# Kernel tuning notes

Hardware: AMD Instinct MI355X
Metric: run time of the kernel (lower is better)

## Reference

```python
import jax, jax.numpy as jnp
import numpy as np

B, N, K, D = 32, 100, 20, 4096
DI = 512   # img_feat_dim
DO = 512   # obj_feat_dim (must equal DI for the module to run)
H = 512    # lstm_hidden_dim
L = 2      # n_hidden_layers


def _w(key, shape, fan_in):
    return (jax.random.normal(key, shape, jnp.float32) / np.sqrt(fan_in)).astype(jnp.float32)


def setup_inputs() -> dict:
    key = jax.random.key(0)
    ks = jax.random.split(key, 24)
    inp = {
        "x": jax.random.normal(ks[0], (B, N, K, D), jnp.float32),
        # feature linears
        "W_img": _w(ks[1], (DI, D), D), "b_img": jnp.zeros((DI,), jnp.float32),
        "W_obj": _w(ks[2], (DO, D), D), "b_obj": jnp.zeros((DO,), jnp.float32),
        "W_obj2": _w(ks[3], (DI, DO), DO), "b_obj2": jnp.zeros((DI,), jnp.float32),
        # Fattn (no biases)
        "W_ah": _w(ks[4], (DI, H), H),   # hidden_linear: H -> DI
        "W_ac": _w(ks[5], (1, DI), DI),  # combined_linear: DI -> 1
        # LSTM layer 0 (input 2*DI) and layer 1 (input H); PyTorch gate order i,f,g,o
        "W_ih0": _w(ks[6], (4 * H, DI + DO), DI + DO), "W_hh0": _w(ks[7], (4 * H, H), H),
        "b_ih0": jnp.zeros((4 * H,), jnp.float32), "b_hh0": jnp.zeros((4 * H,), jnp.float32),
        "W_ih1": _w(ks[8], (4 * H, H), H), "W_hh1": _w(ks[9], (4 * H, H), H),
        "b_ih1": jnp.zeros((4 * H,), jnp.float32), "b_hh1": jnp.zeros((4 * H,), jnp.float32),
        # output head
        "W_out": _w(ks[10], (1, H), H), "b_out": jnp.zeros((1,), jnp.float32),
    }
    return inp


def _forward(x, W_img, b_img, W_obj, b_obj, W_obj2, b_obj2, W_ah, W_ac,
             W_ih0, W_hh0, b_ih0, b_hh0, W_ih1, W_hh1, b_ih1, b_hh1, W_out, b_out):
    Bx, Nx, Kx, Dx = x.shape
    # obj_mask: (B, N, K-1, 1)
    obj_mask = jnp.sum(x[:, :, 1:], axis=-1, keepdims=True)
    img_feat = x[:, :, 0, :] @ W_img.T + b_img                      # (B, N, DI)
    obj_feat = (x[:, :, 1:, :] @ W_obj.T + b_obj) * obj_mask        # (B, N, K-1, DO)
    obj_feat = obj_feat @ W_obj2.T + b_obj2                         # (B, N, K-1, DI)

    lstm_params = ((W_ih0, W_hh0, b_ih0, b_hh0), (W_ih1, W_hh1, b_ih1, b_hh1))

    def step(carry, inp):
        h, c, prev = carry                 # h,c: (L,B,H); prev: (B,H) = top-layer output
        a, im, m = inp                     # a:(B,K-1,DI) im:(B,DI) m:(B,K-1,1)
        # Fattn: note softmax over a size-1 axis -> ones; kept for faithfulness
        hprime = (prev @ W_ah.T)[:, None, :]                        # (B,1,DI)
        e = jnp.tanh(hprime + a)
        al = e @ W_ac.T                                             # (B,K-1,1)
        al = jax.nn.softmax(al, axis=-1) * m                        # == m
        w_obj = jnp.sum(a * al, axis=1)                             # (B,DI)
        xl = jnp.concatenate([im, w_obj], axis=1)                   # (B, DI+DO)
        hs, cs = [], []
        for l, (Wih, Whh, bih, bhh) in enumerate(lstm_params):
            g = xl @ Wih.T + bih + h[l] @ Whh.T + bhh
            gi, gf, gg, go = jnp.split(g, 4, axis=-1)
            cn = jax.nn.sigmoid(gf) * c[l] + jax.nn.sigmoid(gi) * jnp.tanh(gg)
            hn = jax.nn.sigmoid(go) * jnp.tanh(cn)
            hs.append(hn); cs.append(cn); xl = hn
        h = jnp.stack(hs); c = jnp.stack(cs)
        pred = xl @ W_out.T + b_out                                 # (B,1)
        return (h, c, xl), (al, pred[:, 0])

    h0 = jnp.zeros((L, Bx, H), x.dtype)
    c0 = jnp.zeros_like(h0)
    p0 = jnp.zeros((Bx, H), x.dtype)
    xs = (obj_feat.transpose(1, 0, 2, 3), img_feat.transpose(1, 0, 2),
          obj_mask.transpose(1, 0, 2, 3))
    _, (alphas, preds) = jax.lax.scan(step, (h0, c0, p0), xs)
    # alphas: (N, B, K-1, 1) (torch returns a list of N); preds -> (B, N) like torch.cat dim=1
    return alphas, preds.T


def reference(x, W_img, b_img, W_obj, b_obj, W_obj2, b_obj2, W_ah, W_ac,
              W_ih0, W_hh0, b_ih0, b_hh0, W_ih1, W_hh1, b_ih1, b_hh1, W_out, b_out):
    return _forward(x, W_img, b_img, W_obj, b_obj, W_obj2, b_obj2, W_ah, W_ac,
                    W_ih0, W_hh0, b_ih0, b_hh0, W_ih1, W_hh1, b_ih1, b_hh1, W_out, b_out)
```

## Files before the change

### kernel.cpp

```cpp
#include <hip/hip_runtime.h>


__device__ __forceinline__ float sigf(float x) { return 1.0f / (1.0f + __expf(-x)); }

__global__ __launch_bounds__(256) void mask_z_kernel(
    const float* __restrict__ x, float* __restrict__ z,
    float* __restrict__ s1, float* __restrict__ s2, float* __restrict__ alphas)
{
  int m = blockIdx.x;
  int b = m / 100, n = m % 100;
  int t = threadIdx.x;
  const float* xb = x + (size_t)m * 81920;
  __shared__ float red[4];
  float zv[16];
#pragma unroll
  for (int i = 0; i < 16; ++i) zv[i] = 0.f;
  float s1v = 0.f, s2v = 0.f;
  for (int k = 1; k < 20; ++k) {
    const float4* row = (const float4*)(xb + (size_t)k * 4096);
    float4 v0 = row[t], v1 = row[t + 256], v2 = row[t + 512], v3 = row[t + 768];
    float ps = v0.x + v0.y + v0.z + v0.w + v1.x + v1.y + v1.z + v1.w
             + v2.x + v2.y + v2.z + v2.w + v3.x + v3.y + v3.z + v3.w;
#pragma unroll
    for (int off = 32; off >= 1; off >>= 1) ps += __shfl_down(ps, off);
    if ((t & 63) == 0) red[t >> 6] = ps;
    __syncthreads();
    float mk = red[0] + red[1] + red[2] + red[3];
    __syncthreads();
    float mk2 = mk * mk;
    s1v += mk; s2v += mk2;
    if (t == 0) alphas[((size_t)n * 32 + (size_t)b) * 19 + (k - 1)] = mk;
    zv[0] += mk2 * v0.x; zv[1] += mk2 * v0.y; zv[2] += mk2 * v0.z; zv[3] += mk2 * v0.w;
    zv[4] += mk2 * v1.x; zv[5] += mk2 * v1.y; zv[6] += mk2 * v1.z; zv[7] += mk2 * v1.w;
    zv[8] += mk2 * v2.x; zv[9] += mk2 * v2.y; zv[10] += mk2 * v2.z; zv[11] += mk2 * v2.w;
    zv[12] += mk2 * v3.x; zv[13] += mk2 * v3.y; zv[14] += mk2 * v3.z; zv[15] += mk2 * v3.w;
  }
  float4* zr = (float4*)(z + (size_t)m * 4096);
  zr[t]       = make_float4(zv[0], zv[1], zv[2], zv[3]);
  zr[t + 256] = make_float4(zv[4], zv[5], zv[6], zv[7]);
  zr[t + 512] = make_float4(zv[8], zv[9], zv[10], zv[11]);
  zr[t + 768] = make_float4(zv[12], zv[13], zv[14], zv[15]);
  if (t == 0) { s1[m] = s1v; s2[m] = s2v; }
}

__global__ void colvec_kernel(const float* __restrict__ W2,
                              const float* __restrict__ bo, float* __restrict__ vb)
{
  int j = blockIdx.x * 256 + threadIdx.x;
  if (j < 512) {
    float s = 0.f;
    for (int i = 0; i < 512; ++i) s += W2[(size_t)j * 512 + i] * bo[i];
    vb[j] = s;
  }
}

__global__ __launch_bounds__(256) void gemm_atb(
    const float* __restrict__ A, int lda,
    const float* __restrict__ W, int K,
    float* __restrict__ C, int ldc,
    const float* __restrict__ bias1, const float* __restrict__ bias2,
    const float* __restrict__ rs1, const float* __restrict__ cv1,
    const float* __restrict__ rs2, const float* __restrict__ cv2)
{
  __shared__ __align__(16) float As[32 * 76];
  __shared__ __align__(16) float Ws[32 * 76];
  int t = threadIdx.x;
  int m0 = blockIdx.x * 64, n0 = blockIdx.y * 64;
  int sr = t >> 3;
  int sc = t & 7;
  int r0 = (t >> 4) * 4, c0 = (t & 15) * 4;

  float acc[4][4];
#pragma unroll
  for (int i = 0; i < 4; ++i)
#pragma unroll
    for (int j = 0; j < 4; ++j) acc[i][j] = 0.f;

  const float* Ap0 = A + (size_t)(m0 + sr) * lda + sc * 4;
  const float* Ap1 = A + (size_t)(m0 + sr + 32) * lda + sc * 4;
  const float* Wp0 = W + (size_t)(n0 + sr) * K + sc * 4;
  const float* Wp1 = W + (size_t)(n0 + sr + 32) * K + sc * 4;

  float4 a0 = *(const float4*)(Ap0);
  float4 a1 = *(const float4*)(Ap1);
  float4 w0 = *(const float4*)(Wp0);
  float4 w1 = *(const float4*)(Wp1);

  for (int k0 = 0; k0 < K; k0 += 32) {
    int kb = sc * 4;
#pragma unroll
    for (int j = 0; j < 4; ++j) {
      float aj0 = (j == 0) ? a0.x : (j == 1) ? a0.y : (j == 2) ? a0.z : a0.w;
      float aj1 = (j == 0) ? a1.x : (j == 1) ? a1.y : (j == 2) ? a1.z : a1.w;
      float wj0 = (j == 0) ? w0.x : (j == 1) ? w0.y : (j == 2) ? w0.z : w0.w;
      float wj1 = (j == 0) ? w1.x : (j == 1) ? w1.y : (j == 2) ? w1.z : w1.w;
      As[(kb + j) * 76 + sr]      = aj0;
      As[(kb + j) * 76 + sr + 32] = aj1;
      Ws[(kb + j) * 76 + sr]      = wj0;
      Ws[(kb + j) * 76 + sr + 32] = wj1;
    }
    __syncthreads();
    if (k0 + 32 < K) {
      a0 = *(const float4*)(Ap0 + k0 + 32);
      a1 = *(const float4*)(Ap1 + k0 + 32);
      w0 = *(const float4*)(Wp0 + k0 + 32);
      w1 = *(const float4*)(Wp1 + k0 + 32);
    }
#pragma unroll 8
    for (int kk = 0; kk < 32; ++kk) {
      float4 av = *(const float4*)&As[kk * 76 + r0];
      float4 wv = *(const float4*)&Ws[kk * 76 + c0];
      float ar[4] = {av.x, av.y, av.z, av.w};
      float wr[4] = {wv.x, wv.y, wv.z, wv.w};
#pragma unroll
      for (int i = 0; i < 4; ++i)
#pragma unroll
        for (int j = 0; j < 4; ++j) acc[i][j] += ar[i] * wr[j];
    }
    __syncthreads();
  }
#pragma unroll
  for (int i = 0; i < 4; ++i) {
    int m = m0 + r0 + i;
    float r1v = rs1 ? rs1[m] : 0.f;
    float r2v = rs2 ? rs2[m] : 0.f;
#pragma unroll
    for (int j = 0; j < 4; ++j) {
      int n = n0 + c0 + j;
      float v = acc[i][j];
      if (bias1) v += bias1[n];
      if (bias2) v += bias2[n];
      if (cv1) v += r1v * cv1[n];
      if (cv2) v += r2v * cv2[n];
      C[(size_t)m * ldc + n] = v;
    }
  }
}

__global__ __launch_bounds__(256) void lstm_phase(
    const float* __restrict__ gin,
    const float* __restrict__ Whh0,
    const float* __restrict__ Wih1,
    const float* __restrict__ Whh1,
    const float* __restrict__ b_ih1, const float* __restrict__ b_hh1,
    const float* __restrict__ Wout, const float* __restrict__ bout,
    const float* __restrict__ hA_prev, const float* __restrict__ cA_prev,
    float* __restrict__ hA_cur, float* __restrict__ cA_cur,
    const float* __restrict__ h1_prev, const float* __restrict__ c1_prev,
    float* __restrict__ h1_cur, float* __restrict__ c1_cur,
    float* __restrict__ preds, int p)
{
  __shared__ __align__(16) float lds[8 * 1024 + 1024];
  int bid = blockIdx.x, t = threadIdx.x;
  bool isA = bid < 256;
  int wg = isA ? bid : bid - 256;

  {
    int r = t >> 5, c = t & 31;
    int grow = (r >> 1) * 512 + wg * 2 + (r & 1);
    if (isA) {
      const float4* src = (const float4*)(Whh0 + (size_t)grow * 512);
#pragma unroll
      for (int i = 0; i < 4; ++i) {
        int k4 = i * 32 + c;
        *(float4*)&lds[r * 512 + ((k4 ^ r) << 2)] = src[k4];
      }
    } else {
      const float4* sih = (const float4*)(Wih1 + (size_t)grow * 512);
      const float4* shh = (const float4*)(Whh1 + (size_t)grow * 512);
#pragma unroll
      for (int i = 0; i < 8; ++i) {
        int k4g = i * 32 + c;
        int half = k4g >> 7;
        int k4 = k4g & 127;
        float4 v = half ? shh[k4] : sih[k4];
        *(float4*)&lds[r * 1024 + half * 512 + ((k4 ^ r) << 2)] = v;
      }
    }
  }
  __syncthreads();

  bool active = isA ? (p <= 99) : (p >= 1 && p <= 100);
  int tc = t & 7, bg = (t >> 3) & 7, ks = t >> 6;
  int b0 = bg * 4;
  float a0 = 0.f, a1 = 0.f, a2 = 0.f, a3 = 0.f;

  if (active) {
    if (isA) {
      int base = tc * 512;
      const float* h = hA_prev;
#pragma unroll 4
      for (int kk = 0; kk < 32; ++kk) {
        int k4 = ks * 32 + kk;
        float4 w = *(const float4*)&lds[base + ((k4 ^ tc) << 2)];
        const float* hp = h + k4 * 4;
        float4 h0v = *(const float4*)(hp + (b0 + 0) * 512);
        float4 h1v = *(const float4*)(hp + (b0 + 1) * 512);
        float4 h2v = *(const float4*)(hp + (b0 + 2) * 512);
        float4 h3v = *(const float4*)(hp + (b0 + 3) * 512);
        a0 += w.x * h0v.x + w.y * h0v.y + w.z * h0v.z + w.w * h0v.w;
        a1 += w.x * h1v.x + w.y * h1v.y + w.z * h1v.z + w.w * h1v.w;
        a2 += w.x * h2v.x + w.y * h2v.y + w.z * h2v.z + w.w * h2v.w;
        a3 += w.x * h3v.x + w.y * h3v.y + w.z * h3v.z + w.w * h3v.w;
      }
    } else {
      int half = ks >> 1;
      const float* xv = half ? h1_prev : hA_prev;
      int base = tc * 1024 + half * 512;
#pragma unroll 4
      for (int kk = 0; kk < 64; ++kk) {
        int k4 = (ks & 1) * 64 + kk;
        float4 w = *(const float4*)&lds[base + ((k4 ^ tc) << 2)];
        const float* hp = xv + k4 * 4;
        float4 h0v = *(const float4*)(hp + (b0 + 0) * 512);
        float4 h1v = *(const float4*)(hp + (b0 + 1) * 512);
        float4 h2v = *(const float4*)(hp + (b0 + 2) * 512);
        float4 h3v = *(const float4*)(hp + (b0 + 3) * 512);
        a0 += w.x * h0v.x + w.y * h0v.y + w.z * h0v.z + w.w * h0v.w;
        a1 += w.x * h1v.x + w.y * h1v.y + w.z * h1v.z + w.w * h1v.w;
        a2 += w.x * h2v.x + w.y * h2v.y + w.z * h2v.z + w.w * h2v.w;
        a3 += w.x * h3v.x + w.y * h3v.y + w.z * h3v.z + w.w * h3v.w;
      }
    }
  }
  float* scratch = lds + 8192;
  if (active && ks > 0) {
    float* sp = scratch + (t - 64) * 4;
    sp[0] = a0; sp[1] = a1; sp[2] = a2; sp[3] = a3;
  }
  __syncthreads();
  if (active && t < 64) {
    a0 += scratch[t * 4 + 0] + scratch[(t + 64) * 4 + 0] + scratch[(t + 128) * 4 + 0];
    a1 += scratch[t * 4 + 1] + scratch[(t + 64) * 4 + 1] + scratch[(t + 128) * 4 + 1];
    a2 += scratch[t * 4 + 2] + scratch[(t + 64) * 4 + 2] + scratch[(t + 128) * 4 + 2];
    a3 += scratch[t * 4 + 3] + scratch[(t + 64) * 4 + 3] + scratch[(t + 128) * 4 + 3];
    int grow = (tc >> 1) * 512 + wg * 2 + (tc & 1);
    if (isA) {
      size_t gi = ((size_t)b0 * 100 + (size_t)p) * 2048 + grow;
      a0 += gin[gi];
      a1 += gin[gi + 204800];
      a2 += gin[gi + 409600];
      a3 += gin[gi + 614400];
    } else {
      float bb = b_ih1[grow] + b_hh1[grow];
      a0 += bb; a1 += bb; a2 += bb; a3 += bb;
    }
    float* gbuf = lds + 8960;
    gbuf[tc * 32 + b0 + 0] = a0;
    gbuf[tc * 32 + b0 + 1] = a1;
    gbuf[tc * 32 + b0 + 2] = a2;
    gbuf[tc * 32 + b0 + 3] = a3;
  }
  __syncthreads();
  if (active && t < 64) {
    const float* gbuf = lds + 8960;
    int u = t & 1, b = t >> 1;
    float giv = gbuf[(0 + u) * 32 + b];
    float gfv = gbuf[(2 + u) * 32 + b];
    float ggv = gbuf[(4 + u) * 32 + b];
    float gov = gbuf[(6 + u) * 32 + b];
    int gu = wg * 2 + u;
    float cp = (isA ? cA_prev : c1_prev)[b * 512 + gu];
    float cn = sigf(gfv) * cp + sigf(giv) * tanhf(ggv);
    float hn = sigf(gov) * tanhf(cn);
    if (isA) { cA_cur[b * 512 + gu] = cn; hA_cur[b * 512 + gu] = hn; }
    else     { c1_cur[b * 512 + gu] = cn; h1_cur[b * 512 + gu] = hn; }
  }
  if (bid == 0 && p >= 2) {
    __syncthreads();
    float* sc = lds + 8192;
    int b = t & 31, k8 = t >> 5;
    const float* hp = h1_prev + b * 512 + k8 * 64;
    const float* wp = Wout + k8 * 64;
    float s = 0.f;
#pragma unroll
    for (int i = 0; i < 64; ++i) s += hp[i] * wp[i];
    sc[k8 * 32 + b] = s;
    __syncthreads();
    if (t < 32) {
      float acc = bout[0];
#pragma unroll
      for (int k8i = 0; k8i < 8; ++k8i) acc += sc[k8i * 32 + t];
      preds[t * 100 + (p - 2)] = acc;
    }
  }
}

extern "C" void kernel_launch(void* const* d_in, const int* in_sizes, int n_in,
                              void* d_out, int out_size, void* d_ws, size_t ws_size,
                              hipStream_t stream) {
  (void)in_sizes; (void)n_in; (void)out_size; (void)ws_size;
  const float* x      = (const float*)d_in[0];
  const float* W_img  = (const float*)d_in[1];
  const float* b_img  = (const float*)d_in[2];
  const float* W_obj  = (const float*)d_in[3];
  const float* b_obj  = (const float*)d_in[4];
  const float* W_obj2 = (const float*)d_in[5];
  const float* b_obj2 = (const float*)d_in[6];
  const float* W_ih0  = (const float*)d_in[9];
  const float* W_hh0  = (const float*)d_in[10];
  const float* b_ih0  = (const float*)d_in[11];
  const float* b_hh0  = (const float*)d_in[12];
  const float* W_ih1  = (const float*)d_in[13];
  const float* W_hh1  = (const float*)d_in[14];
  const float* b_ih1  = (const float*)d_in[15];
  const float* b_hh1  = (const float*)d_in[16];
  const float* W_out  = (const float*)d_in[17];
  const float* b_out  = (const float*)d_in[18];

  float* out    = (float*)d_out;
  float* alphas = out;
  float* preds  = out + 60800;

  float* ws  = (float*)d_ws;
  float* z   = ws;
  float* zW  = z + 13107200;
  float* xl  = zW + 1638400;
  float* gin = xl + 3276800;
  float* s1  = gin + 6553600;
  float* s2  = s1 + 3200;
  float* vb  = s2 + 3200;
  float* st  = vb + 512;
  float* H0[2] = { st + 0 * 16384, st + 1 * 16384 };
  float* C0[2] = { st + 2 * 16384, st + 3 * 16384 };
  float* H1[2] = { st + 4 * 16384, st + 5 * 16384 };
  float* C1[2] = { st + 6 * 16384, st + 7 * 16384 };

  hipMemsetAsync(st, 0, 8 * 16384 * sizeof(float), stream);

  mask_z_kernel<<<3200, 256, 0, stream>>>(x, z, s1, s2, alphas);
  colvec_kernel<<<2, 256, 0, stream>>>(W_obj2, b_obj, vb);
  gemm_atb<<<dim3(50, 8), 256, 0, stream>>>(x, 81920, W_img, 4096, xl, 1024,
      b_img, nullptr, nullptr, nullptr, nullptr, nullptr);
  gemm_atb<<<dim3(50, 8), 256, 0, stream>>>(z, 4096, W_obj, 4096, zW, 512,
      nullptr, nullptr, nullptr, nullptr, nullptr, nullptr);
  gemm_atb<<<dim3(50, 8), 256, 0, stream>>>(zW, 512, W_obj2, 512, xl + 512, 1024,
      nullptr, nullptr, s2, vb, s1, b_obj2);
  gemm_atb<<<dim3(50, 32), 256, 0, stream>>>(xl, 1024, W_ih0, 1024, gin, 2048,
      b_ih0, b_hh0, nullptr, nullptr, nullptr, nullptr);

  for (int p = 0; p <= 101; ++p) {
    const float* haP = H0[(p + 1) & 1];
    const float* caP = C0[(p + 1) & 1];
    float* haC = H0[p & 1];
    float* caC = C0[p & 1];
    const float* h1P = H1[p & 1];
    const float* c1P = C1[p & 1];
    float* h1C = H1[(p + 1) & 1];
    float* c1C = C1[(p + 1) & 1];
    lstm_phase<<<512, 256, 0, stream>>>(gin, W_hh0, W_ih1, W_hh1, b_ih1, b_hh1,
        W_out, b_out, haP, caP, haC, caC, h1P, c1P, h1C, c1C, preds, p);
  }
}
```

Baseline: 2.656 ms.

## Replace per-step LSTM launches with persistent kernel using flag-based dataflow sync

```diff
diff --git a/kernel.cpp b/kernel.cpp
--- a/kernel.cpp
+++ b/kernel.cpp
@@ -1,7 +1,15 @@
 #include <hip/hip_runtime.h>
 
 
+#define NSTEP 100
+
 __device__ __forceinline__ float sigf(float x) { return 1.0f / (1.0f + __expf(-x)); }
+__device__ __forceinline__ int ld_acq(const int* p) {
+  return __hip_atomic_load(p, __ATOMIC_ACQUIRE, __HIP_MEMORY_SCOPE_AGENT);
+}
+__device__ __forceinline__ void st_rel(int* p, int v) {
+  __hip_atomic_store(p, v, __ATOMIC_RELEASE, __HIP_MEMORY_SCOPE_AGENT);
+}
 
 __global__ __launch_bounds__(256) void mask_z_kernel(
     const float* __restrict__ x, float* __restrict__ z,
@@ -137,18 +145,16 @@
   }
 }
 
-__global__ __launch_bounds__(256) void lstm_phase(
+__global__ __launch_bounds__(256) void lstm_persist(
     const float* __restrict__ gin,
     const float* __restrict__ Whh0,
     const float* __restrict__ Wih1,
     const float* __restrict__ Whh1,
     const float* __restrict__ b_ih1, const float* __restrict__ b_hh1,
     const float* __restrict__ Wout, const float* __restrict__ bout,
-    const float* __restrict__ hA_prev, const float* __restrict__ cA_prev,
-    float* __restrict__ hA_cur, float* __restrict__ cA_cur,
-    const float* __restrict__ h1_prev, const float* __restrict__ c1_prev,
-    float* __restrict__ h1_cur, float* __restrict__ c1_cur,
-    float* __restrict__ preds, int p)
+    float* __restrict__ h0_all, float* __restrict__ h1_all,
+    int* __restrict__ flags0, int* __restrict__ flags1,
+    float* __restrict__ preds)
 {
   __shared__ __align__(16) float lds[8 * 1024 + 1024];
   int bid = blockIdx.x, t = threadIdx.x;
@@ -180,108 +186,152 @@
   }
   __syncthreads();
 
-  bool active = isA ? (p <= 99) : (p >= 1 && p <= 100);
   int tc = t & 7, bg = (t >> 3) & 7, ks = t >> 6;
   int b0 = bg * 4;
-  float a0 = 0.f, a1 = 0.f, a2 = 0.f, a3 = 0.f;
-
-  if (active) {
+  float c_reg = 0.f;
+
+  for (int p = 0; p < NSTEP; ++p) {
     if (isA) {
-      int base = tc * 512;
-      const float* h = hA_prev;
+      if (p > 0) {
+        const int* f = flags0 + (size_t)(p - 1) * 256;
+        while (!__syncthreads_and(ld_acq(&f[t]) != 0)) __builtin_amdgcn_s_sleep(8);
+      }
+    } else {
+      const int* f0 = flags0 + (size_t)p * 256;
+      const int* f1 = flags1 + (size_t)(p - 1) * 256;
+      for (;;) {
+        int ok = (ld_acq(&f0[t]) != 0) && (p == 0 || ld_acq(&f1[t]) != 0);
+        if (__syncthreads_and(ok)) break;
+        __builtin_amdgcn_s_sleep(8);
+      }
+      if (bid == 256 && p > 0) {
+        const float* hp_ = h1_all + (size_t)(p - 1) * 16384;
+        float* sc = lds + 8192;
+        int b = t & 31, k8 = t >> 5;
+        const float* hh = hp_ + b * 512 + k8 * 64;
+        const float* wp = Wout + k8 * 64;
+        float s = 0.f;
+#pragma unroll
+        for (int i = 0; i < 64; ++i) s += hh[i] * wp[i];
+        sc[k8 * 32 + b] = s;
+        __syncthreads();
+        if (t < 32) {
+          float acc = bout[0];
+#pragma unroll
+          for (int k8i = 0; k8i < 8; ++k8i) acc += sc[k8i * 32 + t];
+          preds[t * 100 + (p - 1)] = acc;
+        }
+        __syncthreads();
+      }
+    }
+
+    float a0 = 0.f, a1 = 0.f, a2 = 0.f, a3 = 0.f;
+    if (isA) {
+      if (p > 0) {
+        const float* h = h0_all + (size_t)(p - 1) * 16384;
+        int base = tc * 512;
 #pragma unroll 4
-      for (int kk = 0; kk < 32; ++kk) {
-        int k4 = ks * 32 + kk;
-        float4 w = *(const float4*)&lds[base + ((k4 ^ tc) << 2)];
-        const float* hp = h + k4 * 4;
-        float4 h0v = *(const float4*)(hp + (b0 + 0) * 512);
-        float4 h1v = *(const float4*)(hp + (b0 + 1) * 512);
-        float4 h2v = *(const float4*)(hp + (b0 + 2) * 512);
-        float4 h3v = *(const float4*)(hp + (b0 + 3) * 512);
-        a0 += w.x * h0v.x + w.y * h0v.y + w.z * h0v.z + w.w * h0v.w;
-        a1 += w.x * h1v.x + w.y * h1v.y + w.z * h1v.z + w.w * h1v.w;
-        a2 += w.x * h2v.x + w.y * h2v.y + w.z * h2v.z + w.w * h2v.w;
-        a3 += w.x * h3v.x + w.y * h3v.y + w.z * h3v.z + w.w * h3v.w;
+        for (int kk = 0; kk < 32; ++kk) {
+          int k4 = ks * 32 + kk;
+          float4 w = *(const float4*)&lds[base + ((k4 ^ tc) << 2)];
+          const float* hp = h + k4 * 4;
+          float4 h0v = *(const float4*)(hp + (b0 + 0) * 512);
+          float4 h1v = *(const float4*)(hp + (b0 + 1) * 512);
+          float4 h2v = *(const float4*)(hp + (b0 + 2) * 512);
+          float4 h3v = *(const float4*)(hp + (b0 + 3) * 512);
+          a0 += w.x * h0v.x + w.y * h0v.y + w.z * h0v.z + w.w * h0v.w;
+          a1 += w.x * h1v.x + w.y * h1v.y + w.z * h1v.z + w.w * h1v.w;
+          a2 += w.x * h2v.x + w.y * h2v.y + w.z * h2v.z + w.w * h2v.w;
+          a3 += w.x * h3v.x + w.y * h3v.y + w.z * h3v.z + w.w * h3v.w;
+        }
       }
     } else {
       int half = ks >> 1;
-      const float* xv = half ? h1_prev : hA_prev;
-      int base = tc * 1024 + half * 512;
+      const float* xv = half ? (p > 0 ? h1_all + (size_t)(p - 1) * 16384 : nullptr)
+                             : h0_all + (size_t)p * 16384;
+      if (xv) {
+        int base = tc * 1024 + half * 512;
 #pragma unroll 4
-      for (int kk = 0; kk < 64; ++kk) {
-        int k4 = (ks & 1) * 64 + kk;
-        float4 w = *(const float4*)&lds[base + ((k4 ^ tc) << 2)];
-        const float* hp = xv + k4 * 4;
-        float4 h0v = *(const float4*)(hp + (b0 + 0) * 512);
-        float4 h1v = *(const float4*)(hp + (b0 + 1) * 512);
-        float4 h2v = *(const float4*)(hp + (b0 + 2) * 512);
-        float4 h3v = *(const float4*)(hp + (b0 + 3) * 512);
-        a0 += w.x * h0v.x + w.y * h0v.y + w.z * h0v.z + w.w * h0v.w;
-        a1 += w.x * h1v.x + w.y * h1v.y + w.z * h1v.z + w.w * h1v.w;
-        a2 += w.x * h2v.x + w.y * h2v.y + w.z * h2v.z + w.w * h2v.w;
-        a3 += w.x * h3v.x + w.y * h3v.y + w.z * h3v.z + w.w * h3v.w;
-      }
-    }
-  }
-  float* scratch = lds + 8192;
-  if (active && ks > 0) {
-    float* sp = scratch + (t - 64) * 4;
-    sp[0] = a0; sp[1] = a1; sp[2] = a2; sp[3] = a3;
-  }
-  __syncthreads();
-  if (active && t < 64) {
-    a0 += scratch[t * 4 + 0] + scratch[(t + 64) * 4 + 0] + scratch[(t + 128) * 4 + 0];
-    a1 += scratch[t * 4 + 1] + scratch[(t + 64) * 4 + 1] + scratch[(t + 128) * 4 + 1];
-    a2 += scratch[t * 4 + 2] + scratch[(t + 64) * 4 + 2] + scratch[(t + 128) * 4 + 2];
-    a3 += scratch[t * 4 + 3] + scratch[(t + 64) * 4 + 3] + scratch[(t + 128) * 4 + 3];
-    int grow = (tc >> 1) * 512 + wg * 2 + (tc & 1);
-    if (isA) {
-      size_t gi = ((size_t)b0 * 100 + (size_t)p) * 2048 + grow;
-      a0 += gin[gi];
-      a1 += gin[gi + 204800];
-      a2 += gin[gi + 409600];
-      a3 += gin[gi + 614400];
-    } else {
-      float bb = b_ih1[grow] + b_hh1[grow];
-      a0 += bb; a1 += bb; a2 += bb; a3 += bb;
-    }
-    float* gbuf = lds + 8960;
-    gbuf[tc * 32 + b0 + 0] = a0;
-    gbuf[tc * 32 + b0 + 1] = a1;
-    gbuf[tc * 32 + b0 + 2] = a2;
-    gbuf[tc * 32 + b0 + 3] = a3;
-  }
-  __syncthreads();
-  if (active && t < 64) {
-    const float* gbuf = lds + 8960;
-    int u = t & 1, b = t >> 1;
-    float giv = gbuf[(0 + u) * 32 + b];
-    float gfv = gbuf[(2 + u) * 32 + b];
-    float ggv = gbuf[(4 + u) * 32 + b];
-    float gov = gbuf[(6 + u) * 32 + b];
-    int gu = wg * 2 + u;
-    float cp = (isA ? cA_prev : c1_prev)[b * 512 + gu];
-    float cn = sigf(gfv) * cp + sigf(giv) * tanhf(ggv);
-    float hn = sigf(gov) * tanhf(cn);
-    if (isA) { cA_cur[b * 512 + gu] = cn; hA_cur[b * 512 + gu] = hn; }
-    else     { c1_cur[b * 512 + gu] = cn; h1_cur[b * 512 + gu] = hn; }
-  }
-  if (bid == 0 && p >= 2) {
-    __syncthreads();
+        for (int kk = 0; kk < 64; ++kk) {
+          int k4 = (ks & 1) * 64 + kk;
+          float4 w = *(const float4*)&lds[base + ((k4 ^ tc) << 2)];
+          const float* hp = xv + k4 * 4;
+          float4 h0v = *(const float4*)(hp + (b0 + 0) * 512);
+          float4 h1v = *(const float4*)(hp + (b0 + 1) * 512);
+          float4 h2v = *(const float4*)(hp + (b0 + 2) * 512);
+          float4 h3v = *(const float4*)(hp + (b0 + 3) * 512);
+          a0 += w.x * h0v.x + w.y * h0v.y + w.z * h0v.z + w.w * h0v.w;
+          a1 += w.x * h1v.x + w.y * h1v.y + w.z * h1v.z + w.w * h1v.w;
+          a2 += w.x * h2v.x + w.y * h2v.y + w.z * h2v.z + w.w * h2v.w;
+          a3 += w.x * h3v.x + w.y * h3v.y + w.z * h3v.z + w.w * h3v.w;
+        }
+      }
+    }
+
+    float* scratch = lds + 8192;
+    if (ks > 0) {
+      float* sp = scratch + (t - 64) * 4;
+      sp[0] = a0; sp[1] = a1; sp[2] = a2; sp[3] = a3;
+    }
+    __syncthreads();
+    if (t < 64) {
+      a0 += scratch[t * 4 + 0] + scratch[(t + 64) * 4 + 0] + scratch[(t + 128) * 4 + 0];
+      a1 += scratch[t * 4 + 1] + scratch[(t + 64) * 4 + 1] + scratch[(t + 128) * 4 + 1];
+      a2 += scratch[t * 4 + 2] + scratch[(t + 64) * 4 + 2] + scratch[(t + 128) * 4 + 2];
+      a3 += scratch[t * 4 + 3] + scratch[(t + 64) * 4 + 3] + scratch[(t + 128) * 4 + 3];
+      int grow = (tc >> 1) * 512 + wg * 2 + (tc & 1);
+      if (isA) {
+        size_t gi = ((size_t)b0 * 100 + (size_t)p) * 2048 + grow;
+        a0 += gin[gi];
+        a1 += gin[gi + 204800];
+        a2 += gin[gi + 409600];
+        a3 += gin[gi + 614400];
+      } else {
+        float bb = b_ih1[grow] + b_hh1[grow];
+        a0 += bb; a1 += bb; a2 += bb; a3 += bb;
+      }
+      float* gbuf = lds + 8960;
+      gbuf[tc * 32 + b0 + 0] = a0;
+      gbuf[tc * 32 + b0 + 1] = a1;
+      gbuf[tc * 32 + b0 + 2] = a2;
+      gbuf[tc * 32 + b0 + 3] = a3;
+    }
+    __syncthreads();
+    if (t < 64) {
+      const float* gbuf = lds + 8960;
+      int u = t & 1, b = t >> 1;
+      float giv = gbuf[(0 + u) * 32 + b];
+      float gfv = gbuf[(2 + u) * 32 + b];
+      float ggv = gbuf[(4 + u) * 32 + b];
+      float gov = gbuf[(6 + u) * 32 + b];
+      float cn = sigf(gfv) * c_reg + sigf(giv) * tanhf(ggv);
+      float hn = sigf(gov) * tanhf(cn);
+      c_reg = cn;
+      float* hdst = (isA ? h0_all : h1_all) + (size_t)p * 16384;
+      hdst[b * 512 + wg * 2 + u] = hn;
+    }
+    __syncthreads();
+    if (t == 0) st_rel((isA ? flags0 : flags1) + (size_t)p * 256 + wg, 1);
+  }
+
+  if (bid == 256) {
+    const int* f1 = flags1 + (size_t)99 * 256;
+    while (!__syncthreads_and(ld_acq(&f1[t]) != 0)) __builtin_amdgcn_s_sleep(8);
+    const float* hp_ = h1_all + (size_t)99 * 16384;
     float* sc = lds + 8192;
     int b = t & 31, k8 = t >> 5;
-    const float* hp = h1_prev + b * 512 + k8 * 64;
+    const float* hh = hp_ + b * 512 + k8 * 64;
     const float* wp = Wout + k8 * 64;
     float s = 0.f;
 #pragma unroll
-    for (int i = 0; i < 64; ++i) s += hp[i] * wp[i];
+    for (int i = 0; i < 64; ++i) s += hh[i] * wp[i];
     sc[k8 * 32 + b] = s;
     __syncthreads();
     if (t < 32) {
       float acc = bout[0];
 #pragma unroll
       for (int k8i = 0; k8i < 8; ++k8i) acc += sc[k8i * 32 + t];
-      preds[t * 100 + (p - 2)] = acc;
+      preds[t * 100 + 99] = acc;
     }
   }
 }
@@ -312,21 +362,20 @@
   float* alphas = out;
   float* preds  = out + 60800;
 
-  float* ws  = (float*)d_ws;
-  float* z   = ws;
-  float* zW  = z + 13107200;
-  float* xl  = zW + 1638400;
-  float* gin = xl + 3276800;
-  float* s1  = gin + 6553600;
-  float* s2  = s1 + 3200;
-  float* vb  = s2 + 3200;
-  float* st  = vb + 512;
-  float* H0[2] = { st + 0 * 16384, st + 1 * 16384 };
-  float* C0[2] = { st + 2 * 16384, st + 3 * 16384 };
-  float* H1[2] = { st + 4 * 16384, st + 5 * 16384 };
-  float* C1[2] = { st + 6 * 16384, st + 7 * 16384 };
-
-  hipMemsetAsync(st, 0, 8 * 16384 * sizeof(float), stream);
+  float* ws     = (float*)d_ws;
+  float* z      = ws;
+  float* zW     = z + 13107200;
+  float* xl     = zW + 1638400;
+  float* gin    = xl + 3276800;
+  float* s1     = gin + 6553600;
+  float* s2     = s1 + 3200;
+  float* vb     = s2 + 3200;
+  float* h0_all = vb + 512;
+  float* h1_all = h0_all + 1638400;
+  int*   flags0 = (int*)(h1_all + 1638400);
+  int*   flags1 = flags0 + 25600;
+
+  hipMemsetAsync(flags0, 0, 2 * 25600 * sizeof(int), stream);
 
   mask_z_kernel<<<3200, 256, 0, stream>>>(x, z, s1, s2, alphas);
   colvec_kernel<<<2, 256, 0, stream>>>(W_obj2, b_obj, vb);
@@ -339,16 +388,6 @@
   gemm_atb<<<dim3(50, 32), 256, 0, stream>>>(xl, 1024, W_ih0, 1024, gin, 2048,
       b_ih0, b_hh0, nullptr, nullptr, nullptr, nullptr);
 
-  for (int p = 0; p <= 101; ++p) {
-    const float* haP = H0[(p + 1) & 1];
-    const float* caP = C0[(p + 1) & 1];
-    float* haC = H0[p & 1];
-    float* caC = C0[p & 1];
-    const float* h1P = H1[p & 1];
-    const float* c1P = C1[p & 1];
-    float* h1C = H1[(p + 1) & 1];
-    float* c1C = C1[(p + 1) & 1];
-    lstm_phase<<<512, 256, 0, stream>>>(gin, W_hh0, W_ih1, W_hh1, b_ih1, b_hh1,
-        W_out, b_out, haP, caP, haC, caC, h1P, c1P, h1C, c1C, preds, p);
-  }
-}
+  lstm_persist<<<512, 256, 0, stream>>>(gin, W_hh0, W_ih1, W_hh1, b_ih1, b_hh1,
+      W_out, b_out, h0_all, h1_all, flags0, flags1, preds);
+}
```

New measurement: 8.641 ms. +225.3%, slower.
